# Optimization experiments

Measured on AMD Instinct MI355X. Metric: run time of the kernel, lower is better.

The kernel has to match this reference:

```python
import jax, jax.numpy as jnp
import numpy as np

SIGMAS = (2.5, 4.0, 6.0, 9.0, 14.0)
TRUNCATE = 4.0
POOL = 16
COND_HIDDEN = 32


def _gauss_kernel_bank():
    """All K Gaussian kernels zero-padded (center-aligned) to a common length.
    Zero padding a centered symmetric kernel does not change the conv result,
    so a single grouped conv computes all K depthwise smoothings at once.
    Returns kernel bank [K, 1, L] and the common half-width pad."""
    ks = []
    for s in SIGMAS:
        r = max(1, int(TRUNCATE * s))
        xs = np.arange(-r, r + 1, dtype=np.float32)
        k = np.exp(-0.5 * (xs / s) ** 2)
        k = k / (k.sum() + 1e-12)
        ks.append(k)
    L = max(len(k) for k in ks)  # 113 for default sigmas
    bank = np.zeros((len(ks), 1, L), np.float32)
    for i, k in enumerate(ks):
        off = (L - len(k)) // 2
        bank[i, 0, off:off + len(k)] = k
    return jnp.asarray(bank), (L - 1) // 2


def setup_inputs() -> dict:
    key = jax.random.key(0)
    k0, k1, k2 = jax.random.split(key, 3)
    B, T, C = 16, 4096, 256
    H, K = COND_HIDDEN, len(SIGMAS)
    return {
        "x": jax.random.normal(k0, (B, T, C), jnp.float32),
        "W1": jax.random.normal(k1, (3, H), jnp.float32) * 0.5,
        "b1": jnp.zeros((H,), jnp.float32),
        "W2": jax.random.normal(k2, (H, K), jnp.float32) * 0.2,
        "b2": jnp.zeros((K,), jnp.float32),
    }


def reference(x, W1, b1, W2, b2):
    B, T, C = x.shape
    bank, pad = _gauss_kernel_bank()  # [K,1,L]
    # K depthwise Gaussian convs, fused into one grouped conv by treating
    # each (batch, channel) pair as an independent conv batch element.
    xin = x.transpose(0, 2, 1).reshape(B * C, 1, T)  # [B*C,1,T]
    y = jax.lax.conv_general_dilated(xin, bank, (1,), [(pad, pad)])  # [B*C,K,T]
    Y = y.reshape(B, C, -1, T).transpose(0, 3, 1, 2)  # [B,T,C,K]

    # local mean / variance with reflect padding (matches F.pad mode='reflect')
    pL = (POOL - 1) // 2
    pR = POOL - 1 - pL
    xp = jnp.pad(x, ((0, 0), (pL, pR), (0, 0)), mode="reflect")  # [B,T+POOL-1,C]
    cs = jnp.cumsum(xp, axis=1)
    cs = jnp.concatenate([jnp.zeros_like(cs[:, :1]), cs], axis=1)
    mean = (cs[:, POOL:] - cs[:, :-POOL]) / POOL  # [B,T,C]
    cs2 = jnp.cumsum(xp * xp, axis=1)
    cs2 = jnp.concatenate([jnp.zeros_like(cs2[:, :1]), cs2], axis=1)
    mean2 = (cs2[:, POOL:] - cs2[:, :-POOL]) / POOL
    var = jnp.maximum(mean2 - mean * mean, 0.0)

    # tiny per-position conditioner MLP -> softmax mixture weights over K
    feats = jnp.stack([mean, var, x], axis=-1)  # [B,T,C,3]
    h = jax.nn.gelu(feats @ W1 + b1, approximate=False)  # torch GELU = exact erf
    logits = h @ W2 + b2  # [B,T,C,K]
    w = jax.nn.softmax(logits, axis=-1)
    return (Y * w).sum(axis=-1)  # [B,T,C]
```

## Files before the change

### kernel.cpp

```cpp
#include <hip/hip_runtime.h>
#include <math.h>

#define T_LEN 4096
#define C_LEN 256
#define B_LEN 16
#define LOG2E 1.4426950408889634f
#define HSTR 80
#define LSTR 12

constexpr double cexp(double x) {
    double y = x * (1.0 / 1024.0);
    double t = 1.0, term = 1.0;
    for (int i = 1; i <= 12; ++i) { term *= y / i; t += term; }
    for (int i = 0; i < 10; ++i) t = t * t;
    return t;
}

constexpr int RAD[5] = {10, 16, 24, 36, 56};

struct Bank { float g[5][57]; };

constexpr Bank make_bank() {
    Bank b{};
    const double sig[5] = {2.5, 4.0, 6.0, 9.0, 14.0};
    for (int k = 0; k < 5; ++k) {
        double w[57] = {};
        for (int j = 0; j <= RAD[k]; ++j)
            w[j] = cexp(-0.5 * (double)(j * j) / (sig[k] * sig[k]));
        double s = w[0];
        for (int j = 1; j <= RAD[k]; ++j) s += 2.0 * w[j];
        s += 1e-12;
        for (int j = 0; j <= RAD[k]; ++j) b.g[k][j] = (float)(w[j] / s);
    }
    return b;
}

constexpr Bank BANK = make_bank();

typedef _Float16 hf;
typedef hf    hfx2 __attribute__((ext_vector_type(2)));
typedef hf    hfx8 __attribute__((ext_vector_type(8)));
typedef float f32x4 __attribute__((ext_vector_type(4)));

__device__ __forceinline__ void lds_fence() { asm volatile("" ::: "memory"); }

__device__ __forceinline__ float fast_exp2(float x) {
#if __has_builtin(__builtin_amdgcn_exp2f)
    return __builtin_amdgcn_exp2f(x);
#else
    return __expf(x * 0.6931471805599453f);
#endif
}

__device__ __forceinline__ float gelu_fast(float v) {
    const float c1 = (float)(-2.0 * 0.7978845608028654 * 1.4426950408889634);
    const float c2 = c1 * 0.044715f;
    float v2 = v * v;
    float t  = fmaf(c2, v2, c1);
    float z  = v * t;
    float e  = fast_exp2(z);
    float r  = __builtin_amdgcn_rcpf(1.0f + e);
    return v * r;
}

__device__ __forceinline__ float ldz(const float* __restrict__ xb, int tt) {
    if (tt < 0 || tt >= T_LEN) return 0.0f;
    return xb[tt * C_LEN];
}

struct Frags { hfx8 b1a, b1b, b2; f32x4 c2; };

__device__ __forceinline__ Frags build_frags(const float* __restrict__ wraw, int lane) {
    Frags f;
    const int n = lane & 15, g = lane >> 4;
    hfx8 z = {0, 0, 0, 0, 0, 0, 0, 0};
    f.b1a = z; f.b1b = z;
    if (g == 0) {
        f.b1a[0] = (hf)wraw[n];      f.b1b[0] = (hf)wraw[16 + n];
        f.b1a[1] = (hf)wraw[32 + n]; f.b1b[1] = (hf)wraw[48 + n];
        f.b1a[2] = (hf)wraw[64 + n]; f.b1b[2] = (hf)wraw[80 + n];
        f.b1a[3] = (hf)wraw[96 + n]; f.b1b[3] = (hf)wraw[112 + n];
    }
#pragma unroll
    for (int j = 0; j < 8; ++j) {
        int kk = 8 * g + j;
        int canon = ((kk & 1) << 4) | (kk >> 1);
        float wv = (n < 5) ? wraw[128 + canon * 5 + n] * LOG2E : 0.0f;
        f.b2[j] = (hf)wv;
    }
    float cc = (n < 5) ? wraw[288 + n] * LOG2E : 0.0f;
    f.c2 = (f32x4){cc, cc, cc, cc};
    return f;
}

template <bool CHECKED>
__device__ __forceinline__ void work(const float* __restrict__ x,
                                     float* __restrict__ out,
                                     const float* __restrict__ wraw,
                                     char* __restrict__ fe,
                                     char* __restrict__ hb,
                                     char* __restrict__ lgb,
                                     int b, int t0, int c, int lane) {
    const float* xb = x + (size_t)b * T_LEN * C_LEN + c;

    float v[19];
#pragma unroll
    for (int i = 0; i < 19; ++i) {
        int tt = t0 - 7 + i;
        if (CHECKED) {
            tt = (tt < 0) ? -tt : tt;
            tt = (tt >= T_LEN) ? (2 * T_LEN - 2 - tt) : tt;
        }
        v[i] = xb[tt * C_LEN];
    }

    float mean[4], var[4], xc[4];
    {
        float s = 0.f, q = 0.f;
#pragma unroll
        for (int i = 0; i < 16; ++i) { s += v[i]; q = fmaf(v[i], v[i], q); }
#pragma unroll
        for (int m = 0; m < 4; ++m) {
            if (m > 0) {
                float nw = v[15 + m], od = v[m - 1];
                s = s + nw - od;
                q = fmaf(nw, nw, fmaf(od, -od, q));
            }
            mean[m] = s * 0.0625f;
            float m2 = q * 0.0625f;
            float vv = fmaf(-mean[m], mean[m], m2);
            var[m] = vv > 0.f ? vv : 0.f;
            xc[m]  = v[7 + m];
        }
    }

#pragma unroll
    for (int m = 0; m < 4; ++m) {
        auto p0 = __builtin_amdgcn_cvt_pkrtz(mean[m], var[m]);
        auto p1 = __builtin_amdgcn_cvt_pkrtz(xc[m], 1.0f);
        int4 r4;
        r4.x = __builtin_bit_cast(int, p0);
        r4.y = __builtin_bit_cast(int, p1);
        r4.z = 0; r4.w = 0;
        *(int4*)(fe + (m * 64 + lane) * 16) = r4;
    }
    lds_fence();

    float acc[5][4];
#pragma unroll
    for (int k = 0; k < 5; ++k)
#pragma unroll
        for (int m = 0; m < 4; ++m) acc[k][m] = BANK.g[k][0] * xc[m];

    float F[4], Bw[4];
    if (CHECKED) {
        F[1] = ldz(xb, t0 + 1); F[2] = ldz(xb, t0 + 2);
        F[3] = ldz(xb, t0 + 3); F[0] = ldz(xb, t0 + 4);
        Bw[3] = ldz(xb, t0 - 1); Bw[0] = ldz(xb, t0);
        Bw[1] = ldz(xb, t0 + 1); Bw[2] = ldz(xb, t0 + 2);
    } else {
        F[1] = v[8]; F[2] = v[9]; F[3] = v[10]; F[0] = v[11];
        Bw[3] = v[6]; Bw[0] = v[7]; Bw[1] = v[8]; Bw[2] = v[9];
    }

#pragma unroll
    for (int j = 1; j <= 56; ++j) {
        float sm[4];
#pragma unroll
        for (int m = 0; m < 4; ++m)
            sm[m] = F[(j + m) & 3] + Bw[(m - j) & 3];
#pragma unroll
        for (int k = 0; k < 5; ++k) {
            if (j <= RAD[k]) {
#pragma unroll
                for (int m = 0; m < 4; ++m)
                    acc[k][m] = fmaf(BANK.g[k][j], sm[m], acc[k][m]);
            }
        }
        if (j < 56) {
            if (CHECKED) {
                F[j & 3]        = ldz(xb, t0 + j + 4);
                Bw[(3 - j) & 3] = ldz(xb, t0 - j - 1);
            } else {
                F[j & 3]        = (j <= 7) ? v[j + 11] : xb[(t0 + j + 4) * C_LEN];
                Bw[(3 - j) & 3] = (j <= 6) ? v[6 - j]  : xb[(t0 - j - 1) * C_LEN];
            }
        }
    }

    Frags fr = build_frags(wraw, lane);
    const int rl = lane & 15, gq = lane >> 4;
    const char* a1p = fe + rl * 16;
    char*       hwp = hb + gq * (4 * HSTR) + rl * 4;
    const char* a2p = hb + rl * HSTR + gq * 16;
    char*       lwp = lgb + (4 * gq) * LSTR + rl * 2;
    const f32x4 z4 = (f32x4){0.f, 0.f, 0.f, 0.f};

#pragma unroll 2
    for (int t = 0; t < 16; ++t) {
        hfx8 a1 = *(const hfx8*)(a1p + t * 256);
        f32x4 d1a = __builtin_amdgcn_mfma_f32_16x16x32_f16(a1, fr.b1a, z4, 0, 0, 0);
        f32x4 d1b = __builtin_amdgcn_mfma_f32_16x16x32_f16(a1, fr.b1b, z4, 0, 0, 0);
#pragma unroll
        for (int r = 0; r < 4; ++r) {
            auto hp = __builtin_amdgcn_cvt_pkrtz(gelu_fast(d1a[r]), gelu_fast(d1b[r]));
            *(int*)(hwp + r * HSTR) = __builtin_bit_cast(int, hp);
        }
        lds_fence();
        hfx8 a2 = *(const hfx8*)a2p;
        lds_fence();
        f32x4 d2 = __builtin_amdgcn_mfma_f32_16x16x32_f16(a2, fr.b2, fr.c2, 0, 0, 0);
        if (rl < 5) {
#pragma unroll
            for (int r = 0; r < 4; ++r)
                *(hf*)(lwp + (t * 16 + r) * LSTR) = (hf)d2[r];
        }
    }
    lds_fence();

#pragma unroll
    for (int m = 0; m < 4; ++m) {
        const char* Lr = lgb + (m * 64 + lane) * LSTR;
        int  w01 = *(const int*)(Lr);
        int  w23 = *(const int*)(Lr + 4);
        hf   q4  = *(const hf*)(Lr + 8);
        hfx2 q01 = __builtin_bit_cast(hfx2, w01);
        hfx2 q23 = __builtin_bit_cast(hfx2, w23);
        float e0 = fast_exp2((float)q01[0]);
        float e1 = fast_exp2((float)q01[1]);
        float e2 = fast_exp2((float)q23[0]);
        float e3 = fast_exp2((float)q23[1]);
        float e4 = fast_exp2((float)q4);
        float den = ((e0 + e1) + (e2 + e3)) + e4;
        float num = e0 * acc[0][m];
        num = fmaf(e1, acc[1][m], num);
        num = fmaf(e2, acc[2][m], num);
        num = fmaf(e3, acc[3][m], num);
        num = fmaf(e4, acc[4][m], num);
        out[((size_t)b * T_LEN + t0 + m) * C_LEN + c] = num * __builtin_amdgcn_rcpf(den);
    }
}

__global__ __launch_bounds__(256, 2) void agt_fused(
    const float* __restrict__ x, const float* __restrict__ W1,
    const float* __restrict__ b1, const float* __restrict__ W2,
    const float* __restrict__ b2, float* __restrict__ out) {
    __shared__ float wraw[296];
    __shared__ __align__(16) char fe_lds[4][4096];
    __shared__ __align__(16) char h_lds[4][16 * HSTR];
    __shared__ __align__(16) char lg_lds[4][256 * LSTR];

    int tid = threadIdx.x;
    for (int i = tid; i < 293; i += 256) {
        float w;
        if (i < 96)       w = W1[i];
        else if (i < 128) w = b1[i - 96];
        else if (i < 288) w = W2[i - 128];
        else              w = b2[i - 288];
        wraw[i] = w;
    }
    __syncthreads();

    int b     = blockIdx.x >> 10;
    int chunk = blockIdx.x & 1023;
    int t0    = chunk * 4;
    int lane  = tid & 63;
    char* fe  = &fe_lds[tid >> 6][0];
    char* hb  = &h_lds[tid >> 6][0];
    char* lgb = &lg_lds[tid >> 6][0];

    if (chunk >= 14 && chunk < 1010)
        work<false>(x, out, wraw, fe, hb, lgb, b, t0, tid, lane);
    else
        work<true>(x, out, wraw, fe, hb, lgb, b, t0, tid, lane);
}

extern "C" void kernel_launch(void* const* d_in, const int* in_sizes, int n_in,
                              void* d_out, int out_size, void* d_ws, size_t ws_size,
                              hipStream_t stream) {
    const float* x  = (const float*)d_in[0];
    const float* W1 = (const float*)d_in[1];
    const float* b1 = (const float*)d_in[2];
    const float* W2 = (const float*)d_in[3];
    const float* b2 = (const float*)d_in[4];
    float* out = (float*)d_out;

    (void)in_sizes; (void)n_in; (void)d_ws; (void)ws_size; (void)out_size;

    agt_fused<<<dim3(B_LEN * 1024), dim3(256), 0, stream>>>(x, W1, b1, W2, b2, out);
}
```

Before: 462.4 us.

## Feed MLP A-fragments via ds_bpermute and double-buffer hidden tile

Drops the per-wave 4KB feature staging buffer in LDS. The packed mean/var/x fragments now stay in registers and are routed to MFMA A-operand lanes with ds_bpermute. The hidden-activation buffer is double-buffered so the layer-1 MFMA and GELU for tile t+1 run while layer 2 reads tile t, which leaves one LDS fence per iteration instead of two. Intended gains are less LDS traffic and footprint, fewer barriers and more overlap, at the cost of extra registers from full unrolling and bpermute latency.

```diff
diff --git a/kernel.cpp b/kernel.cpp
--- a/kernel.cpp
+++ b/kernel.cpp
@@ -6,6 +6,7 @@
 #define B_LEN 16
 #define LOG2E 1.4426950408889634f
 #define HSTR 80
+#define HBUF (16 * HSTR)
 #define LSTR 12
 
 constexpr double cexp(double x) {
@@ -97,7 +98,6 @@
 __device__ __forceinline__ void work(const float* __restrict__ x,
                                      float* __restrict__ out,
                                      const float* __restrict__ wraw,
-                                     char* __restrict__ fe,
                                      char* __restrict__ hb,
                                      char* __restrict__ lgb,
                                      int b, int t0, int c, int lane) {
@@ -134,17 +134,12 @@
         }
     }
 
+    int pk0[4], pk1[4];
 #pragma unroll
     for (int m = 0; m < 4; ++m) {
-        auto p0 = __builtin_amdgcn_cvt_pkrtz(mean[m], var[m]);
-        auto p1 = __builtin_amdgcn_cvt_pkrtz(xc[m], 1.0f);
-        int4 r4;
-        r4.x = __builtin_bit_cast(int, p0);
-        r4.y = __builtin_bit_cast(int, p1);
-        r4.z = 0; r4.w = 0;
-        *(int4*)(fe + (m * 64 + lane) * 16) = r4;
-    }
-    lds_fence();
+        pk0[m] = __builtin_bit_cast(int, __builtin_amdgcn_cvt_pkrtz(mean[m], var[m]));
+        pk1[m] = __builtin_bit_cast(int, __builtin_amdgcn_cvt_pkrtz(xc[m], 1.0f));
+    }
 
     float acc[5][4];
 #pragma unroll
@@ -189,27 +184,64 @@
     }
 
     Frags fr = build_frags(wraw, lane);
-    const int rl = lane & 15, gq = lane >> 4;
-    const char* a1p = fe + rl * 16;
-    char*       hwp = hb + gq * (4 * HSTR) + rl * 4;
-    const char* a2p = hb + rl * HSTR + gq * 16;
-    char*       lwp = lgb + (4 * gq) * LSTR + rl * 2;
+    const int rl  = lane & 15, gq = lane >> 4;
+    const int rl4 = rl * 4;
+    char* const hw_base = hb + gq * (4 * HSTR) + rl * 4;
+    const char* const a2_base = hb + rl * HSTR + gq * 16;
+    char* const lwp = lgb + (4 * gq) * LSTR + rl * 2;
     const f32x4 z4 = (f32x4){0.f, 0.f, 0.f, 0.f};
 
-#pragma unroll 2
-    for (int t = 0; t < 16; ++t) {
-        hfx8 a1 = *(const hfx8*)(a1p + t * 256);
+    int ib0[2], ib1[2];
+
+    ib0[0] = __builtin_amdgcn_ds_bpermute(rl4, pk0[0]);
+    ib1[0] = __builtin_amdgcn_ds_bpermute(rl4, pk1[0]);
+    {
+        int4 t4; t4.x = ib0[0]; t4.y = ib1[0]; t4.z = 0; t4.w = 0;
+        hfx8 a1 = __builtin_bit_cast(hfx8, t4);
         f32x4 d1a = __builtin_amdgcn_mfma_f32_16x16x32_f16(a1, fr.b1a, z4, 0, 0, 0);
         f32x4 d1b = __builtin_amdgcn_mfma_f32_16x16x32_f16(a1, fr.b1b, z4, 0, 0, 0);
 #pragma unroll
         for (int r = 0; r < 4; ++r) {
             auto hp = __builtin_amdgcn_cvt_pkrtz(gelu_fast(d1a[r]), gelu_fast(d1b[r]));
-            *(int*)(hwp + r * HSTR) = __builtin_bit_cast(int, hp);
+            *(int*)(hw_base + r * HSTR) = __builtin_bit_cast(int, hp);
+        }
+    }
+    ib0[1] = __builtin_amdgcn_ds_bpermute(rl4 + 64, pk0[0]);
+    ib1[1] = __builtin_amdgcn_ds_bpermute(rl4 + 64, pk1[0]);
+    lds_fence();
+
+#pragma unroll
+    for (int t = 0; t < 16; ++t) {
+        hfx8 a2 = *(const hfx8*)(a2_base + (t & 1) * HBUF);
+
+        f32x4 d1a, d1b;
+        if (t < 15) {
+            const int j = t + 1;
+            int4 t4; t4.x = ib0[j & 1]; t4.y = ib1[j & 1]; t4.z = 0; t4.w = 0;
+            hfx8 a1 = __builtin_bit_cast(hfx8, t4);
+            d1a = __builtin_amdgcn_mfma_f32_16x16x32_f16(a1, fr.b1a, z4, 0, 0, 0);
+            d1b = __builtin_amdgcn_mfma_f32_16x16x32_f16(a1, fr.b1b, z4, 0, 0, 0);
+        }
+
+        if (t < 14) {
+            const int j = t + 2;
+            ib0[j & 1] = __builtin_amdgcn_ds_bpermute(rl4 + 64 * (j & 3), pk0[j >> 2]);
+            ib1[j & 1] = __builtin_amdgcn_ds_bpermute(rl4 + 64 * (j & 3), pk1[j >> 2]);
+        }
+
+        if (t < 15) {
+            const int j = t + 1;
+            char* hw = hw_base + (j & 1) * HBUF;
+#pragma unroll
+            for (int r = 0; r < 4; ++r) {
+                auto hp = __builtin_amdgcn_cvt_pkrtz(gelu_fast(d1a[r]), gelu_fast(d1b[r]));
+                *(int*)(hw + r * HSTR) = __builtin_bit_cast(int, hp);
+            }
         }
         lds_fence();
-        hfx8 a2 = *(const hfx8*)a2p;
-        lds_fence();
+
         f32x4 d2 = __builtin_amdgcn_mfma_f32_16x16x32_f16(a2, fr.b2, fr.c2, 0, 0, 0);
+
         if (rl < 5) {
 #pragma unroll
             for (int r = 0; r < 4; ++r)
@@ -246,8 +278,7 @@
     const float* __restrict__ b1, const float* __restrict__ W2,
     const float* __restrict__ b2, float* __restrict__ out) {
     __shared__ float wraw[296];
-    __shared__ __align__(16) char fe_lds[4][4096];
-    __shared__ __align__(16) char h_lds[4][16 * HSTR];
+    __shared__ __align__(16) char h_lds[4][2 * HBUF];
     __shared__ __align__(16) char lg_lds[4][256 * LSTR];
 
     int tid = threadIdx.x;
@@ -265,14 +296,13 @@
     int chunk = blockIdx.x & 1023;
     int t0    = chunk * 4;
     int lane  = tid & 63;
-    char* fe  = &fe_lds[tid >> 6][0];
     char* hb  = &h_lds[tid >> 6][0];
     char* lgb = &lg_lds[tid >> 6][0];
 
     if (chunk >= 14 && chunk < 1010)
-        work<false>(x, out, wraw, fe, hb, lgb, b, t0, tid, lane);
+        work<false>(x, out, wraw, hb, lgb, b, t0, tid, lane);
     else
-        work<true>(x, out, wraw, fe, hb, lgb, b, t0, tid, lane);
+        work<true>(x, out, wraw, hb, lgb, b, t0, tid, lane);
 }
 
 extern "C" void kernel_launch(void* const* d_in, const int* in_sizes, int n_in,
```

Measured after the change: 455.7 us. About the same (-1.4%).
